# Kernel optimization log

Hardware: AMD Instinct MI355X
Metric: run time of the kernel (lower is better)

The kernel has to match this reference:

```python
import jax, jax.numpy as jnp
import numpy as np

B, N, D, H, O = 8, 2048, 64, 64, 64
ALPHA = 2.0  # LeakyReLU negative slope per module default
NEG = -9e15


def _lin(x, W, b):
    # torch nn.Linear: y = x @ W.T + b, W is [out, in]
    return x @ W.T + b


def setup_inputs() -> dict:
    key = jax.random.key(0)
    ks = jax.random.split(key, 32)
    f32 = jnp.float32
    x = jax.random.normal(ks[0], (B, N, D), f32)
    adj = jax.random.randint(ks[1], (B, N, N), 0, 2).astype(f32)
    c = jax.random.normal(ks[2], (B, N, H), f32)
    h = jax.random.normal(ks[3], (B, N, H), f32)
    s = 0.1
    W = jax.random.normal(ks[4], (D, H), f32) * s           # GAT weight
    a = jax.random.normal(ks[5], (2 * H, 1), f32) * s       # GAT attention vector
    def lin(k, out_d, in_d):
        k1, k2 = jax.random.split(k)
        return (jax.random.normal(k1, (out_d, in_d), f32) * s,
                jax.random.normal(k2, (out_d,), f32) * s)
    Wf, bWf = lin(ks[6], H, H); Wi, bWi = lin(ks[7], H, H)
    Wo, bWo = lin(ks[8], H, H); Wc, bWc = lin(ks[9], H, H)
    Uf, bUf = lin(ks[10], H, D); Ui, bUi = lin(ks[11], H, D)
    Uo, bUo = lin(ks[12], H, D); Uc, bUc = lin(ks[13], H, D)
    Wout, bout = lin(ks[14], O, 2 * H)
    return dict(x=x, adj=adj, c=c, h=h, W=W, a=a,
                Wf=Wf, bWf=bWf, Wi=Wi, bWi=bWi, Wo=Wo, bWo=bWo, Wc=Wc, bWc=bWc,
                Uf=Uf, bUf=bUf, Ui=Ui, bUi=bUi, Uo=Uo, bUo=bUo, Uc=Uc, bUc=bUc,
                Wout=Wout, bout=bout)


def reference(x, adj, c, h, W, a,
              Wf, bWf, Wi, bWi, Wo, bWo, Wc, bWc,
              Uf, bUf, Ui, bUi, Uo, bUo, Uc, bUc,
              Wout, bout):
    # ---- GraphAttentionLayer (eval mode: dropout is identity) ----
    Wh = x @ W                                   # [B,N,H]
    # e[b,i,j] = leakyrelu(a[:H].Wh_i + a[H:].Wh_j) -- same math as the
    a_src = (Wh @ a[:H]).squeeze(-1)             # [B,N]
    a_dst = (Wh @ a[H:]).squeeze(-1)             # [B,N]
    e = jax.nn.leaky_relu(a_src[:, :, None] + a_dst[:, None, :], ALPHA)  # [B,N,N]
    att = jnp.where(adj > 0, e, NEG)
    att = jax.nn.softmax(att, axis=2)
    x_hidden = jax.nn.elu(att @ Wh)              # [B,N,H] (concat=True)
    # ---- LSTMLayer step ----
    f_t = jax.nn.sigmoid(_lin(h, Wf, bWf) + _lin(x, Uf, bUf))
    i_t = jax.nn.sigmoid(_lin(h, Wi, bWi) + _lin(x, Ui, bUi))
    o_t = jax.nn.sigmoid(_lin(h, Wo, bWo) + _lin(x, Uo, bUo))
    c_hat = jnp.tanh(_lin(h, Wc, bWc) + _lin(x, Uc, bUc))
    c_t = f_t * c + i_t * c_hat
    h_t = o_t * jax.nn.relu(c_t)                 # gate = nn.ReLU() default
    total = jnp.concatenate([x_hidden, h_t], axis=2)  # [B,N,2H]
    output = jax.nn.relu(_lin(total, Wout, bout))     # [B,N,O]
    return (output, h_t, c_t)
```

## Files before the change

kernel.cpp:

```cpp
#include <hip/hip_runtime.h>
#include <math.h>

#define B_ 8
#define N_ 2048
#define NT_ (B_*N_)
#define OUTSZ (NT_*64)

#define WS_XH    0
#define WS_ASRC  (WS_XH + NT_*64)
#define WS_ADST  (WS_ASRC + NT_)
#define WS_GMAX  (WS_ADST + NT_)
#define WS_WT    (WS_GMAX + 32)
#define WS_BB    (WS_WT + 128*256)
#define WS_WOT   (WS_BB + 256)
#define WS_DPART (WS_WOT + 128*64)
#define WS_PART  (WS_DPART + 4*NT_)

typedef float f32x4 __attribute__((ext_vector_type(4)));
typedef __bf16 bf16x8 __attribute__((ext_vector_type(8)));
typedef __bf16 bf16x4 __attribute__((ext_vector_type(4)));

__device__ __forceinline__ float lrelu2(float x) { return x > 0.f ? x : 2.f * x; }
__device__ __forceinline__ float f4get(const float4& v, int k) { return k==0?v.x:(k==1?v.y:(k==2?v.z:v.w)); }

__global__ void k0_prep(const float* Wf, const float* Wi, const float* Wo, const float* Wc,
                        const float* Uf, const float* Ui, const float* Uo, const float* Uc,
                        const float* bWf, const float* bWi, const float* bWo, const float* bWc,
                        const float* bUf, const float* bUi, const float* bUo, const float* bUc,
                        const float* Wout, float* ws)
{
    int idx = blockIdx.x * 256 + threadIdx.x;
    if (idx < 128 * 256) {
        int k = idx >> 8, o = idx & 255;
        int g = o >> 6, u = o & 63;
        const float* Wg = (g == 0) ? Wf : (g == 1) ? Wi : (g == 2) ? Wo : Wc;
        const float* Ug = (g == 0) ? Uf : (g == 1) ? Ui : (g == 2) ? Uo : Uc;
        ws[WS_WT + idx] = (k < 64) ? Wg[u * 64 + k] : Ug[u * 64 + (k - 64)];
    } else if (idx < 128 * 256 + 256) {
        int o = idx - 128 * 256;
        int g = o >> 6, u = o & 63;
        const float* bW = (g == 0) ? bWf : (g == 1) ? bWi : (g == 2) ? bWo : bWc;
        const float* bU = (g == 0) ? bUf : (g == 1) ? bUi : (g == 2) ? bUo : bUc;
        ws[WS_BB + o] = bW[u] + bU[u];
    } else if (idx < 128 * 256 + 256 + 128 * 64) {
        int j = idx - (128 * 256 + 256);
        int k = j >> 6, u = j & 63;
        ws[WS_WOT + j] = Wout[u * 128 + k];
    }
}

__global__ __launch_bounds__(256) void k1_wh(const float* __restrict__ x, const float* __restrict__ W,
                                             const float* __restrict__ a, float* __restrict__ ws,
                                             __bf16* __restrict__ whT)
{
    __shared__ float xl[64 * 68];
    __shared__ float Wl[64 * 68];
    int t = threadIdx.x;
    int i0 = blockIdx.x * 64;
    #pragma unroll
    for (int it = 0; it < 4; ++it) {
        int f = t + 256 * it;
        int r = f >> 4, q = f & 15;
        *(float4*)&xl[r * 68 + q * 4] = *(const float4*)&x[i0 * 64 + f * 4];
        *(float4*)&Wl[r * 68 + q * 4] = *(const float4*)&W[f * 4];
    }
    __syncthreads();
    int cg = t & 15, rg = t >> 4;
    int c0 = cg * 4, r0 = rg * 4;
    float acc[4][4] = {};
    #pragma unroll
    for (int d0 = 0; d0 < 64; d0 += 4) {
        float4 wv[4], xv[4];
        #pragma unroll
        for (int k = 0; k < 4; ++k) wv[k] = *(float4*)&Wl[(d0 + k) * 68 + c0];
        #pragma unroll
        for (int ri = 0; ri < 4; ++ri) xv[ri] = *(float4*)&xl[(r0 + ri) * 68 + d0];
        #pragma unroll
        for (int ri = 0; ri < 4; ++ri)
            #pragma unroll
            for (int k = 0; k < 4; ++k) {
                float xs = f4get(xv[ri], k);
                acc[ri][0] += xs * wv[k].x; acc[ri][1] += xs * wv[k].y;
                acc[ri][2] += xs * wv[k].z; acc[ri][3] += xs * wv[k].w;
            }
    }
    int b = i0 >> 11;
    int rowb0 = (i0 & 2047) + r0;
    #pragma unroll
    for (int cj = 0; cj < 4; ++cj) {
        bf16x4 v;
        v[0] = (__bf16)acc[0][cj]; v[1] = (__bf16)acc[1][cj];
        v[2] = (__bf16)acc[2][cj]; v[3] = (__bf16)acc[3][cj];
        *(bf16x4*)&whT[((size_t)(b * 64 + c0 + cj)) * N_ + rowb0] = v;
    }
    float4 a0 = *(const float4*)&a[c0];
    float4 a1 = *(const float4*)&a[64 + c0];
    #pragma unroll
    for (int ri = 0; ri < 4; ++ri) {
        int row = i0 + r0 + ri;
        float s0 = acc[ri][0]*a0.x + acc[ri][1]*a0.y + acc[ri][2]*a0.z + acc[ri][3]*a0.w;
        float s1 = acc[ri][0]*a1.x + acc[ri][1]*a1.y + acc[ri][2]*a1.z + acc[ri][3]*a1.w;
        #pragma unroll
        for (int m = 1; m < 16; m <<= 1) { s0 += __shfl_xor(s0, m, 64); s1 += __shfl_xor(s1, m, 64); }
        if (cg == 0) { ws[WS_ASRC + row] = s0; ws[WS_ADST + row] = s1; }
    }
}

__global__ void k1b_gmax(float* ws)
{
    __shared__ float red[256];
    int b = blockIdx.x, t = threadIdx.x;
    float m = -3.0e38f;
    for (int j = t; j < N_; j += 256) m = fmaxf(m, ws[WS_ADST + b * N_ + j]);
    red[t] = m; __syncthreads();
    for (int s = 128; s > 0; s >>= 1) { if (t < s) red[t] = fmaxf(red[t], red[t + s]); __syncthreads(); }
    if (t == 0) ws[WS_GMAX + b] = red[0];
}

__global__ __launch_bounds__(64) void k2m(const float* __restrict__ adj,
                                          const __bf16* __restrict__ whT,
                                          float* __restrict__ ws, int js_count)
{
    int lane = threadIdx.x;
    int r = lane & 15, g = lane >> 4;
    int blk = blockIdx.x;
    int rb = blk / js_count;
    int js = blk - rb * js_count;
    int row0 = rb * 16;
    int b = row0 >> 11;
    int jlen = N_ / js_count;
    int jbeg = js * jlen;

    float as = ws[WS_ASRC + row0 + r];
    float M = lrelu2(as + ws[WS_GMAX + b]);
    const float* adjrow = &adj[(size_t)(row0 + r) * N_];
    const float* adstp = &ws[WS_ADST + b * N_];
    const __bf16* bb = &whT[((size_t)(b * 64 + r)) * N_];

    f32x4 acc0 = {0.f,0.f,0.f,0.f}, acc1 = {0.f,0.f,0.f,0.f};
    f32x4 acc2 = {0.f,0.f,0.f,0.f}, acc3 = {0.f,0.f,0.f,0.f};
    float dsum = 0.f;

    for (int j0 = jbeg; j0 < jbeg + jlen; j0 += 32) {
        int jk = j0 + g * 8;
        float4 av0 = *(const float4*)&adjrow[jk];
        float4 av1 = *(const float4*)&adjrow[jk + 4];
        float4 d0  = *(const float4*)&adstp[jk];
        float4 d1  = *(const float4*)&adstp[jk + 4];
        float pvv[8];
        #pragma unroll
        for (int e = 0; e < 8; ++e) {
            float a_ = f4get(e < 4 ? av0 : av1, e & 3);
            float dd = f4get(e < 4 ? d0  : d1,  e & 3);
            float s = as + dd;
            float ee = fminf(s, s + s);
            float p_ = (a_ > 0.f) ? __expf(ee - M) : 0.f;
            pvv[e] = p_;
        }
        float ds_ = 0.f;
        #pragma unroll
        for (int e = 0; e < 8; ++e) ds_ += pvv[e];
        dsum += ds_;
        bf16x8 af;
        #pragma unroll
        for (int e = 0; e < 8; ++e) af[e] = (__bf16)pvv[e];
        bf16x8 b0 = *(const bf16x8*)&bb[jk];
        bf16x8 b1 = *(const bf16x8*)&bb[16 * N_ + jk];
        bf16x8 b2 = *(const bf16x8*)&bb[32 * N_ + jk];
        bf16x8 b3 = *(const bf16x8*)&bb[48 * N_ + jk];
        acc0 = __builtin_amdgcn_mfma_f32_16x16x32_bf16(af, b0, acc0, 0, 0, 0);
        acc1 = __builtin_amdgcn_mfma_f32_16x16x32_bf16(af, b1, acc1, 0, 0, 0);
        acc2 = __builtin_amdgcn_mfma_f32_16x16x32_bf16(af, b2, acc2, 0, 0, 0);
        acc3 = __builtin_amdgcn_mfma_f32_16x16x32_bf16(af, b3, acc3, 0, 0, 0);
    }
    dsum += __shfl_xor(dsum, 16, 64);
    dsum += __shfl_xor(dsum, 32, 64);

    if (js_count == 1) {
        float invr[4];
        #pragma unroll
        for (int i = 0; i < 4; ++i) invr[i] = 1.f / __shfl(dsum, g * 4 + i, 64);
        auto fin = [&](f32x4 acc_, int n) {
            #pragma unroll
            for (int i = 0; i < 4; ++i) {
                int row = row0 + g * 4 + i;
                float v = acc_[i] * invr[i];
                v = v > 0.f ? v : expm1f(v);
                ws[WS_XH + (size_t)row * 64 + n * 16 + r] = v;
            }
        };
        fin(acc0, 0); fin(acc1, 1); fin(acc2, 2); fin(acc3, 3);
    } else {
        float* part = &ws[WS_PART + (size_t)js * (NT_ * 64)];
        auto st = [&](f32x4 acc_, int n) {
            #pragma unroll
            for (int i = 0; i < 4; ++i) {
                int row = row0 + g * 4 + i;
                part[(size_t)row * 64 + n * 16 + r] = acc_[i];
            }
        };
        st(acc0, 0); st(acc1, 1); st(acc2, 2); st(acc3, 3);
        if (g == 0) ws[WS_DPART + js * NT_ + row0 + r] = dsum;
    }
}

__global__ __launch_bounds__(256) void k2c(float* __restrict__ ws, int js_count)
{
    int idx = blockIdx.x * 256 + threadIdx.x;
    int row = idx >> 4;
    float4 s = make_float4(0.f, 0.f, 0.f, 0.f);
    float d = 0.f;
    for (int js = 0; js < js_count; ++js) {
        float4 p = *(const float4*)&ws[WS_PART + (size_t)js * (NT_ * 64) + (size_t)idx * 4];
        s.x += p.x; s.y += p.y; s.z += p.z; s.w += p.w;
        d += ws[WS_DPART + js * NT_ + row];
    }
    float inv = 1.f / d;
    float4 o;
    o.x = s.x * inv; o.x = o.x > 0.f ? o.x : expm1f(o.x);
    o.y = s.y * inv; o.y = o.y > 0.f ? o.y : expm1f(o.y);
    o.z = s.z * inv; o.z = o.z > 0.f ? o.z : expm1f(o.z);
    o.w = s.w * inv; o.w = o.w > 0.f ? o.w : expm1f(o.w);
    *(float4*)&ws[WS_XH + (size_t)idx * 4] = o;
}

__global__ __launch_bounds__(256) void k3_lstm(const float* __restrict__ x, const float* __restrict__ c,
                                               const float* __restrict__ h, const float* __restrict__ ws,
                                               float* __restrict__ out)
{
    __shared__ float Al[16 * 132];
    __shared__ float gl[16 * 260];
    int t = threadIdx.x;
    int base = blockIdx.x * 16;
    {
        int r = t >> 4, k0 = (t & 15) * 8;
        const float* src = (k0 < 64) ? &h[(base + r) * 64 + k0] : &x[(base + r) * 64 + (k0 - 64)];
        *(float4*)&Al[r * 132 + k0]     = *(const float4*)&src[0];
        *(float4*)&Al[r * 132 + k0 + 4] = *(const float4*)&src[4];
    }
    __syncthreads();
    int og = t & 63, rg = t >> 6;
    int o0 = og * 4;
    const float* WT = &ws[WS_WT];
    float acc[4][4] = {};
    #pragma unroll
    for (int k0 = 0; k0 < 128; k0 += 4) {
        float4 wv[4], av[4];
        #pragma unroll
        for (int kk = 0; kk < 4; ++kk) wv[kk] = *(const float4*)&WT[(k0 + kk) * 256 + o0];
        #pragma unroll
        for (int rr = 0; rr < 4; ++rr) av[rr] = *(float4*)&Al[(rg + 4 * rr) * 132 + k0];
        #pragma unroll
        for (int rr = 0; rr < 4; ++rr)
            #pragma unroll
            for (int kk = 0; kk < 4; ++kk) {
                float as = f4get(av[rr], kk);
                acc[rr][0] += as * wv[kk].x; acc[rr][1] += as * wv[kk].y;
                acc[rr][2] += as * wv[kk].z; acc[rr][3] += as * wv[kk].w;
            }
    }
    float4 bbv = *(const float4*)&ws[WS_BB + o0];
    #pragma unroll
    for (int rr = 0; rr < 4; ++rr) {
        int r = rg + 4 * rr;
        *(float4*)&gl[r * 260 + o0] = make_float4(acc[rr][0] + bbv.x, acc[rr][1] + bbv.y,
                                                  acc[rr][2] + bbv.z, acc[rr][3] + bbv.w);
    }
    __syncthreads();
    int u = t & 63, rq = t >> 6;
    #pragma unroll
    for (int pp = 0; pp < 4; ++pp) {
        int r = rq + 4 * pp;
        float gf = gl[r * 260 + u];
        float gi = gl[r * 260 + 64 + u];
        float go = gl[r * 260 + 128 + u];
        float gc = gl[r * 260 + 192 + u];
        float fg = 1.f / (1.f + __expf(-gf));
        float ig = 1.f / (1.f + __expf(-gi));
        float oo = 1.f / (1.f + __expf(-go));
        float ch = tanhf(gc);
        float cv = c[(base + r) * 64 + u];
        float ct = fg * cv + ig * ch;
        float ht = oo * fmaxf(ct, 0.f);
        out[OUTSZ + (base + r) * 64 + u] = ht;
        out[2 * OUTSZ + (base + r) * 64 + u] = ct;
    }
}

__global__ __launch_bounds__(256) void k5_out(const float* __restrict__ ws, const float* __restrict__ bout,
                                              float* __restrict__ out)
{
    __shared__ float Al[64 * 132];
    int t = threadIdx.x;
    int base = blockIdx.x * 64;
    const float* xh = &ws[WS_XH];
    const float* ht = &out[OUTSZ];
    #pragma unroll
    for (int it = 0; it < 8; ++it) {
        int f = t + 256 * it;
        int r = f >> 5, q = f & 31;
        int k0 = q * 4;
        float4 v;
        if (k0 < 64) v = *(const float4*)&xh[(base + r) * 64 + k0];
        else         v = *(const float4*)&ht[(base + r) * 64 + (k0 - 64)];
        *(float4*)&Al[r * 132 + k0] = v;
    }
    __syncthreads();
    int cg = t & 15, rgG = t >> 4;
    int c0 = cg * 4, r0 = rgG * 4;
    const float* WT = &ws[WS_WOT];
    float acc[4][4] = {};
    #pragma unroll
    for (int k0 = 0; k0 < 128; k0 += 4) {
        float4 wv[4], av[4];
        #pragma unroll
        for (int kk = 0; kk < 4; ++kk) wv[kk] = *(const float4*)&WT[(k0 + kk) * 64 + c0];
        #pragma unroll
        for (int ri = 0; ri < 4; ++ri) av[ri] = *(float4*)&Al[(r0 + ri) * 132 + k0];
        #pragma unroll
        for (int ri = 0; ri < 4; ++ri)
            #pragma unroll
            for (int kk = 0; kk < 4; ++kk) {
                float as = f4get(av[ri], kk);
                acc[ri][0] += as * wv[kk].x; acc[ri][1] += as * wv[kk].y;
                acc[ri][2] += as * wv[kk].z; acc[ri][3] += as * wv[kk].w;
            }
    }
    float4 bo = *(const float4*)&bout[c0];
    #pragma unroll
    for (int ri = 0; ri < 4; ++ri) {
        int row = base + r0 + ri;
        float4 o;
        o.x = fmaxf(acc[ri][0] + bo.x, 0.f);
        o.y = fmaxf(acc[ri][1] + bo.y, 0.f);
        o.z = fmaxf(acc[ri][2] + bo.z, 0.f);
        o.w = fmaxf(acc[ri][3] + bo.w, 0.f);
        *(float4*)&out[row * 64 + c0] = o;
    }
}

extern "C" void kernel_launch(void* const* d_in, const int* in_sizes, int n_in,
                              void* d_out, int out_size, void* d_ws, size_t ws_size,
                              hipStream_t stream)
{
    const float* x    = (const float*)d_in[0];
    const float* adj  = (const float*)d_in[1];
    const float* c    = (const float*)d_in[2];
    const float* h    = (const float*)d_in[3];
    const float* W    = (const float*)d_in[4];
    const float* a    = (const float*)d_in[5];
    const float* Wf   = (const float*)d_in[6];
    const float* bWf  = (const float*)d_in[7];
    const float* Wi   = (const float*)d_in[8];
    const float* bWi  = (const float*)d_in[9];
    const float* Wo   = (const float*)d_in[10];
    const float* bWo  = (const float*)d_in[11];
    const float* Wc   = (const float*)d_in[12];
    const float* bWc  = (const float*)d_in[13];
    const float* Uf   = (const float*)d_in[14];
    const float* bUf  = (const float*)d_in[15];
    const float* Ui   = (const float*)d_in[16];
    const float* bUi  = (const float*)d_in[17];
    const float* Uo   = (const float*)d_in[18];
    const float* bUo  = (const float*)d_in[19];
    const float* Uc   = (const float*)d_in[20];
    const float* bUc  = (const float*)d_in[21];
    const float* Wout = (const float*)d_in[22];
    const float* bout = (const float*)d_in[23];
    float* out = (float*)d_out;
    float* ws  = (float*)d_ws;
    __bf16* whT = (__bf16*)out;

    size_t wsf = ws_size / sizeof(float);
    int js = 1;
    if ((size_t)WS_PART + 4ull * NT_ * 64 <= wsf) js = 4;
    else if ((size_t)WS_PART + 2ull * NT_ * 64 <= wsf) js = 2;

    k0_prep<<<161, 256, 0, stream>>>(Wf, Wi, Wo, Wc, Uf, Ui, Uo, Uc,
                                     bWf, bWi, bWo, bWc, bUf, bUi, bUo, bUc, Wout, ws);
    k1_wh<<<NT_ / 64, 256, 0, stream>>>(x, W, a, ws, whT);
    k1b_gmax<<<B_, 256, 0, stream>>>(ws);
    k3_lstm<<<NT_ / 16, 256, 0, stream>>>(x, c, h, ws, out);
    k2m<<<(NT_ / 16) * js, 64, 0, stream>>>(adj, whT, ws, js);
    if (js > 1) k2c<<<NT_ * 16 / 256, 256, 0, stream>>>(ws, js);
    k5_out<<<NT_ / 64, 256, 0, stream>>>(ws, bout, out);
}
```

Before: 106.2 us.

## Factor softmax exponentials per-row/per-column and fuse split-K combine into output kernel

```diff
diff --git a/kernel.cpp b/kernel.cpp
--- a/kernel.cpp
+++ b/kernel.cpp
@@ -9,12 +9,16 @@
 #define WS_XH    0
 #define WS_ASRC  (WS_XH + NT_*64)
 #define WS_ADST  (WS_ASRC + NT_)
-#define WS_GMAX  (WS_ADST + NT_)
+#define WS_EJ    (WS_ADST + NT_)
+#define WS_C1    (WS_EJ + NT_)
+#define WS_C2    (WS_C1 + NT_)
+#define WS_THR   (WS_C2 + NT_)
+#define WS_GMAX  (WS_THR + NT_)
 #define WS_WT    (WS_GMAX + 32)
 #define WS_BB    (WS_WT + 128*256)
 #define WS_WOT   (WS_BB + 256)
 #define WS_DPART (WS_WOT + 128*64)
-#define WS_PART  (WS_DPART + 4*NT_)
+#define WS_PART  (WS_DPART + 8*NT_)
 
 typedef float f32x4 __attribute__((ext_vector_type(4)));
 typedef __bf16 bf16x8 __attribute__((ext_vector_type(8)));
@@ -106,68 +110,83 @@
     }
 }
 
-__global__ void k1b_gmax(float* ws)
+__global__ __launch_bounds__(256) void k1b_prep(float* ws)
 {
     __shared__ float red[256];
+    __shared__ float gsh;
     int b = blockIdx.x, t = threadIdx.x;
     float m = -3.0e38f;
-    for (int j = t; j < N_; j += 256) m = fmaxf(m, ws[WS_ADST + b * N_ + j]);
+    for (int j = t; j < N_; j += 256) {
+        float v = ws[WS_ADST + b * N_ + j];
+        ws[WS_EJ + b * N_ + j] = __expf(v);
+        m = fmaxf(m, v);
+    }
     red[t] = m; __syncthreads();
     for (int s = 128; s > 0; s >>= 1) { if (t < s) red[t] = fmaxf(red[t], red[t + s]); __syncthreads(); }
-    if (t == 0) ws[WS_GMAX + b] = red[0];
-}
-
-__global__ __launch_bounds__(64) void k2m(const float* __restrict__ adj,
-                                          const __bf16* __restrict__ whT,
-                                          float* __restrict__ ws, int js_count)
-{
-    int lane = threadIdx.x;
+    if (t == 0) { gsh = red[0]; ws[WS_GMAX + b] = red[0]; }
+    __syncthreads();
+    float gmax = gsh;
+    for (int i = t; i < N_; i += 256) {
+        float as = ws[WS_ASRC + b * N_ + i];
+        float M = lrelu2(as + gmax);
+        ws[WS_C1 + b * N_ + i]  = __expf(as - M);
+        ws[WS_C2 + b * N_ + i]  = __expf(2.f * as - M);
+        ws[WS_THR + b * N_ + i] = __expf(-as);
+    }
+}
+
+__global__ __launch_bounds__(256) void k2m(const float* __restrict__ adj,
+                                           const __bf16* __restrict__ whT,
+                                           float* __restrict__ ws, int js_count)
+{
+    int tid = threadIdx.x;
+    int lane = tid & 63, w = tid >> 6;
+    int nw = blockDim.x >> 6;
     int r = lane & 15, g = lane >> 4;
-    int blk = blockIdx.x;
-    int rb = blk / js_count;
-    int js = blk - rb * js_count;
+    int jpb = js_count / nw;
+    int rb = blockIdx.x / jpb;
+    int jg = blockIdx.x - rb * jpb;
+    int js = jg * nw + w;
     int row0 = rb * 16;
     int b = row0 >> 11;
     int jlen = N_ / js_count;
     int jbeg = js * jlen;
 
-    float as = ws[WS_ASRC + row0 + r];
-    float M = lrelu2(as + ws[WS_GMAX + b]);
-    const float* adjrow = &adj[(size_t)(row0 + r) * N_];
-    const float* adstp = &ws[WS_ADST + b * N_];
-    const __bf16* bb = &whT[((size_t)(b * 64 + r)) * N_];
+    float c1  = ws[WS_C1 + row0 + r];
+    float c2  = ws[WS_C2 + row0 + r];
+    float thr = ws[WS_THR + row0 + r];
+    const float* adjrow = &adj[(size_t)(row0 + r) * N_ + jbeg];
+    const float* ejp    = &ws[WS_EJ + b * N_ + jbeg];
+    const __bf16* bb    = &whT[((size_t)(b * 64 + r)) * N_ + jbeg];
 
     f32x4 acc0 = {0.f,0.f,0.f,0.f}, acc1 = {0.f,0.f,0.f,0.f};
     f32x4 acc2 = {0.f,0.f,0.f,0.f}, acc3 = {0.f,0.f,0.f,0.f};
     float dsum = 0.f;
 
-    for (int j0 = jbeg; j0 < jbeg + jlen; j0 += 32) {
+    for (int j0 = 0; j0 < jlen; j0 += 32) {
         int jk = j0 + g * 8;
         float4 av0 = *(const float4*)&adjrow[jk];
         float4 av1 = *(const float4*)&adjrow[jk + 4];
-        float4 d0  = *(const float4*)&adstp[jk];
-        float4 d1  = *(const float4*)&adstp[jk + 4];
-        float pvv[8];
-        #pragma unroll
-        for (int e = 0; e < 8; ++e) {
-            float a_ = f4get(e < 4 ? av0 : av1, e & 3);
-            float dd = f4get(e < 4 ? d0  : d1,  e & 3);
-            float s = as + dd;
-            float ee = fminf(s, s + s);
-            float p_ = (a_ > 0.f) ? __expf(ee - M) : 0.f;
-            pvv[e] = p_;
-        }
-        float ds_ = 0.f;
-        #pragma unroll
-        for (int e = 0; e < 8; ++e) ds_ += pvv[e];
-        dsum += ds_;
-        bf16x8 af;
-        #pragma unroll
-        for (int e = 0; e < 8; ++e) af[e] = (__bf16)pvv[e];
+        float4 e0  = *(const float4*)&ejp[jk];
+        float4 e1  = *(const float4*)&ejp[jk + 4];
         bf16x8 b0 = *(const bf16x8*)&bb[jk];
         bf16x8 b1 = *(const bf16x8*)&bb[16 * N_ + jk];
         bf16x8 b2 = *(const bf16x8*)&bb[32 * N_ + jk];
         bf16x8 b3 = *(const bf16x8*)&bb[48 * N_ + jk];
+        bf16x8 af;
+        float ds_ = 0.f;
+        #pragma unroll
+        for (int e = 0; e < 8; ++e) {
+            float av = f4get(e < 4 ? av0 : av1, e & 3);
+            float Ej = f4get(e < 4 ? e0  : e1,  e & 3);
+            float pa = c1 * Ej;
+            float pb = c2 * Ej * Ej;
+            float p  = (Ej > thr) ? pa : pb;
+            p = (av > 0.f) ? p : 0.f;
+            ds_ += p;
+            af[e] = (__bf16)p;
+        }
+        dsum += ds_;
         acc0 = __builtin_amdgcn_mfma_f32_16x16x32_bf16(af, b0, acc0, 0, 0, 0);
         acc1 = __builtin_amdgcn_mfma_f32_16x16x32_bf16(af, b1, acc1, 0, 0, 0);
         acc2 = __builtin_amdgcn_mfma_f32_16x16x32_bf16(af, b2, acc2, 0, 0, 0);
@@ -202,26 +221,6 @@
         st(acc0, 0); st(acc1, 1); st(acc2, 2); st(acc3, 3);
         if (g == 0) ws[WS_DPART + js * NT_ + row0 + r] = dsum;
     }
-}
-
-__global__ __launch_bounds__(256) void k2c(float* __restrict__ ws, int js_count)
-{
-    int idx = blockIdx.x * 256 + threadIdx.x;
-    int row = idx >> 4;
-    float4 s = make_float4(0.f, 0.f, 0.f, 0.f);
-    float d = 0.f;
-    for (int js = 0; js < js_count; ++js) {
-        float4 p = *(const float4*)&ws[WS_PART + (size_t)js * (NT_ * 64) + (size_t)idx * 4];
-        s.x += p.x; s.y += p.y; s.z += p.z; s.w += p.w;
-        d += ws[WS_DPART + js * NT_ + row];
-    }
-    float inv = 1.f / d;
-    float4 o;
-    o.x = s.x * inv; o.x = o.x > 0.f ? o.x : expm1f(o.x);
-    o.y = s.y * inv; o.y = o.y > 0.f ? o.y : expm1f(o.y);
-    o.z = s.z * inv; o.z = o.z > 0.f ? o.z : expm1f(o.z);
-    o.w = s.w * inv; o.w = o.w > 0.f ? o.w : expm1f(o.w);
-    *(float4*)&ws[WS_XH + (size_t)idx * 4] = o;
 }
 
 __global__ __launch_bounds__(256) void k3_lstm(const float* __restrict__ x, const float* __restrict__ c,
@@ -288,21 +287,39 @@
 }
 
 __global__ __launch_bounds__(256) void k5_out(const float* __restrict__ ws, const float* __restrict__ bout,
-                                              float* __restrict__ out)
+                                              float* __restrict__ out, int js_count)
 {
     __shared__ float Al[64 * 132];
     int t = threadIdx.x;
     int base = blockIdx.x * 64;
-    const float* xh = &ws[WS_XH];
     const float* ht = &out[OUTSZ];
     #pragma unroll
     for (int it = 0; it < 8; ++it) {
         int f = t + 256 * it;
         int r = f >> 5, q = f & 31;
         int k0 = q * 4;
+        int row = base + r;
         float4 v;
-        if (k0 < 64) v = *(const float4*)&xh[(base + r) * 64 + k0];
-        else         v = *(const float4*)&ht[(base + r) * 64 + (k0 - 64)];
+        if (k0 < 64) {
+            if (js_count == 1) {
+                v = *(const float4*)&ws[WS_XH + (size_t)row * 64 + k0];
+            } else {
+                float4 s = make_float4(0.f, 0.f, 0.f, 0.f);
+                float d = 0.f;
+                for (int js = 0; js < js_count; ++js) {
+                    float4 p = *(const float4*)&ws[WS_PART + (size_t)js * (NT_ * 64) + (size_t)row * 64 + k0];
+                    s.x += p.x; s.y += p.y; s.z += p.z; s.w += p.w;
+                    d += ws[WS_DPART + js * NT_ + row];
+                }
+                float inv = 1.f / d;
+                v.x = s.x * inv; v.x = v.x > 0.f ? v.x : expm1f(v.x);
+                v.y = s.y * inv; v.y = v.y > 0.f ? v.y : expm1f(v.y);
+                v.z = s.z * inv; v.z = v.z > 0.f ? v.z : expm1f(v.z);
+                v.w = s.w * inv; v.w = v.w > 0.f ? v.w : expm1f(v.w);
+            }
+        } else {
+            v = *(const float4*)&ht[(size_t)row * 64 + (k0 - 64)];
+        }
         *(float4*)&Al[r * 132 + k0] = v;
     }
     __syncthreads();
@@ -373,15 +390,18 @@
 
     size_t wsf = ws_size / sizeof(float);
     int js = 1;
-    if ((size_t)WS_PART + 4ull * NT_ * 64 <= wsf) js = 4;
-    else if ((size_t)WS_PART + 2ull * NT_ * 64 <= wsf) js = 2;
+    if ((size_t)WS_PART + 8ull * NT_ * 64 <= wsf) js = 8;
+    else if ((size_t)WS_PART + 4ull * NT_ * 64 <= wsf) js = 4;
 
     k0_prep<<<161, 256, 0, stream>>>(Wf, Wi, Wo, Wc, Uf, Ui, Uo, Uc,
                                      bWf, bWi, bWo, bWc, bUf, bUi, bUo, bUc, Wout, ws);
     k1_wh<<<NT_ / 64, 256, 0, stream>>>(x, W, a, ws, whT);
-    k1b_gmax<<<B_, 256, 0, stream>>>(ws);
+    k1b_prep<<<B_, 256, 0, stream>>>(ws);
     k3_lstm<<<NT_ / 16, 256, 0, stream>>>(x, c, h, ws, out);
-    k2m<<<(NT_ / 16) * js, 64, 0, stream>>>(adj, whT, ws, js);
-    if (js > 1) k2c<<<NT_ * 16 / 256, 256, 0, stream>>>(ws, js);
-    k5_out<<<NT_ / 64, 256, 0, stream>>>(ws, bout, out);
-}
+
+    int thr_ = (js >= 4) ? 256 : 64;
+    int nblk = (NT_ / 16) * js / (thr_ / 64);
+    k2m<<<nblk, thr_, 0, stream>>>(adj, whT, ws, js);
+
+    k5_out<<<NT_ / 64, 256, 0, stream>>>(ws, bout, out, js);
+}
```

After: 127.8 us. +20.4%, slower.
